# Kernel tuning notes

Measured on AMD Instinct MI355X. Metric: run time of the kernel, lower is better.

## Reference

```python
import jax, jax.numpy as jnp
import numpy as np
from jax import lax

B, C, H, W = 64, 384, 28, 28
E, K, R = 3, 2, 8          # num_experts, top_k, lora rank
HID = 4 * C                # ConvNeXt MLP hidden
EPS = 1e-6
SCALING = 8.0 / 8.0        # alpha / r


def setup_inputs() -> dict:
    key = jax.random.key(0)
    ks = jax.random.split(key, 18)
    N = B * H * W
    f32 = jnp.float32
    inp = {
        "x": jax.random.normal(ks[0], (B, C, H, W), f32),
        "conv_w": jax.random.normal(ks[1], (C, 1, 7, 7), f32) * 0.05,
        "conv_b": jax.random.normal(ks[2], (C,), f32) * 0.02,
        "norm_g": 1.0 + jax.random.normal(ks[3], (C,), f32) * 0.02,
        "norm_b": jax.random.normal(ks[4], (C,), f32) * 0.02,
        "dom_g": jax.random.normal(ks[5], (E, C), f32) * 0.02,
        "dom_b": jax.random.normal(ks[6], (E, C), f32) * 0.02,
        "fc1_w": jax.random.normal(ks[7], (C, HID), f32) * (C ** -0.5),
        "fc1_b": jax.random.normal(ks[8], (HID,), f32) * 0.02,
        "fc2_w": jax.random.normal(ks[9], (HID, C), f32) * (HID ** -0.5),
        "fc2_b": jax.random.normal(ks[10], (C,), f32) * 0.02,
        "w_down": jax.random.normal(ks[11], (E, C, R), f32) * (C ** -0.5),
        "w_up": jax.random.normal(ks[12], (E, R, C), f32) * 0.02,
        "gamma": jax.random.normal(ks[13], (C,), f32) * 0.1,
        "routing_weights": jax.nn.softmax(jax.random.normal(ks[14], (B, E), f32), axis=-1),
        "topk_probs": jax.nn.softmax(jax.random.normal(ks[15], (N, K), f32), axis=-1),
        "topk_indices": jax.random.randint(ks[16], (N, K), 0, E),
    }
    return inp


def _forward(x, conv_w, conv_b, norm_g, norm_b, dom_g, dom_b,
             fc1_w, fc1_b, fc2_w, fc2_b, w_down, w_up, gamma,
             routing_weights, topk_probs, topk_indices):
    shortcut = x
    # depthwise 7x7 conv, NCHW, SAME padding
    y = lax.conv_general_dilated(
        x, conv_w, window_strides=(1, 1), padding=((3, 3), (3, 3)),
        feature_group_count=C,
        dimension_numbers=("NCHW", "OIHW", "NCHW"))
    y = y + conv_b[None, :, None, None]
    y = jnp.transpose(y, (0, 2, 3, 1))  # [B, H, W, C] channels-last path

    # ParallelMoELayerNorm: orig LN + sum_i w_i * LN_i(x). All LNs share eps,
    # so normalize once and fuse affine params per-sample.
    mu = jnp.mean(y, axis=-1, keepdims=True)
    var = jnp.mean(jnp.square(y - mu), axis=-1, keepdims=True)
    xhat = (y - mu) * lax.rsqrt(var + EPS)
    g_eff = norm_g[None, :] + routing_weights @ dom_g   # [B, C]
    b_eff = norm_b[None, :] + routing_weights @ dom_b   # [B, C]
    y = xhat * g_eff[:, None, None, :] + b_eff[:, None, None, :]

    # base ConvNeXt MLP (exact GELU, as torch nn.GELU)
    h = jax.nn.gelu(jnp.einsum("bhwc,cf->bhwf", y, fc1_w) + fc1_b,
                    approximate=False)
    orig_out = jnp.einsum("bhwf,fc->bhwc", h, fc2_w) + fc2_b

    # MoE LoRA: dense per-expert rank-8 compute, combined with top-k weights.
    # Equivalent math to the gather/matmul/scatter-add loop in the source.
    y_flat = y.reshape(-1, C)                                   # [N, C]
    down = jnp.einsum("nc,ecr->enr", y_flat, w_down)            # [E, N, R]
    up = jnp.einsum("enr,erc->enc", jax.nn.gelu(down, approximate=False), w_up)
    # combine weights: comb[n, e] = sum_k topk_probs[n, k] * (topk_indices[n,k]==e)
    comb = jnp.sum(jax.nn.one_hot(topk_indices, E, dtype=y.dtype)
                   * topk_probs[..., None], axis=1)             # [N, E]
    moe_out = jnp.einsum("enc,ne->nc", up * SCALING, comb)
    y = orig_out + moe_out.reshape(B, H, W, C)

    y = jnp.transpose(y, (0, 3, 1, 2))  # back to NCHW
    y = gamma[None, :, None, None] * y  # layer scale; drop_path = identity (eval)
    return y + shortcut


def reference(x, conv_w, conv_b, norm_g, norm_b, dom_g, dom_b,
              fc1_w, fc1_b, fc2_w, fc2_b, w_down, w_up, gamma,
              routing_weights, topk_probs, topk_indices):
    return _forward(x, conv_w, conv_b, norm_g, norm_b, dom_g, dom_b,
                    fc1_w, fc1_b, fc2_w, fc2_b, w_down, w_up, gamma,
                    routing_weights, topk_probs, topk_indices)
```

## Files before the change

kernel.cpp:

```cpp
#include <hip/hip_runtime.h>
#include <hip/hip_bf16.h>
#include <cstdint>
#include <cstddef>

constexpr int cB   = 64;
constexpr int cC   = 384;
constexpr int cH   = 28;
constexpr int cW   = 28;
constexpr int cHID = 1536;
constexpr int cNTOK = cB * cH * cW;
constexpr int cKP   = cHID + 32;
constexpr int cCH   = 2;
constexpr int cMR   = cNTOK / cCH;

typedef __attribute__((ext_vector_type(8))) short bf16x8;
typedef __attribute__((ext_vector_type(4))) float f32x4;

__device__ __forceinline__ float gelu_f(float x) {
  float u = 1.5957691216057308f * x * (1.0f + 0.044715f * x * x);
  float e = __expf(-u);
  return x / (1.0f + e);
}

__device__ __forceinline__ float bf16_to_f(unsigned short s) {
  return __uint_as_float(((unsigned)s) << 16);
}
__device__ __forceinline__ unsigned short f_to_bf16(float v) {
  __hip_bfloat16 hb = __float2bfloat16(v);
  return *reinterpret_cast<unsigned short*>(&hb);
}

__device__ __forceinline__ void gload_lds16(const void* g, void* l) {
  __builtin_amdgcn_global_load_lds(
      (const __attribute__((address_space(1))) unsigned int*)g,
      (__attribute__((address_space(3))) unsigned int*)l, 16, 0, 0);
}

__device__ __forceinline__ int xcd_remap(int b, int nwg) {
  int qn = nwg >> 3, rm = nwg & 7;
  int xcd = b & 7, off = b >> 3;
  return (xcd < rm) ? xcd * (qn + 1) + off
                    : rm * (qn + 1) + (xcd - rm) * qn + off;
}

__global__ __launch_bounds__(256) void prep_eff(
    const float* __restrict__ ng, const float* __restrict__ nb,
    const float* __restrict__ dg, const float* __restrict__ db,
    const float* __restrict__ rw, float* __restrict__ geff, float* __restrict__ beff) {
  int i = blockIdx.x * 256 + threadIdx.x;
  if (i >= cB * cC) return;
  int b = i / cC, c = i - b * cC;
  float g = ng[c], bb = nb[c];
#pragma unroll
  for (int e = 0; e < 3; ++e) {
    float r = rw[b * 3 + e];
    g += r * dg[e * cC + c];
    bb += r * db[e * cC + c];
  }
  geff[i] = g;
  beff[i] = bb;
}

__global__ __launch_bounds__(256) void transpose_bf16(
    const float* __restrict__ w, __hip_bfloat16* __restrict__ wt, int R0, int C0) {
  __shared__ float t[64][65];
  int c0 = blockIdx.x * 64, r0 = blockIdx.y * 64;
  for (int i = threadIdx.x; i < 64 * 64; i += 256) {
    int r = i >> 6, c = i & 63;
    t[r][c] = w[(size_t)(r0 + r) * C0 + c0 + c];
  }
  __syncthreads();
  for (int i = threadIdx.x; i < 64 * 64; i += 256) {
    int c = i >> 6, r = i & 63;
    wt[(size_t)(c0 + c) * R0 + r0 + r] = __float2bfloat16(t[r][c]);
  }
}

__global__ __launch_bounds__(256) void build_fc2t(
    const float* __restrict__ fc2w, const float* __restrict__ wu,
    __hip_bfloat16* __restrict__ fc2t) {
  int i = blockIdx.x * 256 + threadIdx.x;
  if (i >= cC * cKP) return;
  int c = i / cKP, k = i - c * cKP;
  float v = 0.f;
  if (k < cHID) v = fc2w[(size_t)k * cC + c];
  else {
    int j = k - cHID;
    if (j < 24) v = wu[(size_t)(j >> 3) * 8 * cC + (size_t)(j & 7) * cC + c];
  }
  fc2t[i] = __float2bfloat16(v);
}

__global__ __launch_bounds__(256) void build_wdt(
    const float* __restrict__ wd, __hip_bfloat16* __restrict__ wdt) {
  int i = blockIdx.x * 256 + threadIdx.x;
  if (i >= 32 * cC) return;
  int j = i / cC, c = i - j * cC;
  float v = 0.f;
  if (j < 24) v = wd[(size_t)(j >> 3) * cC * 8 + (size_t)c * 8 + (j & 7)];
  wdt[i] = __float2bfloat16(v);
}

constexpr int cPL = 4;
__global__ __launch_bounds__(128) void conv_dw(
    const float* __restrict__ x, const float* __restrict__ cw,
    const float* __restrict__ cb, __hip_bfloat16* __restrict__ out) {
  int pb = blockIdx.x * cPL;
  int c0 = pb % cC;
  __shared__ __align__(16) float tile[cPL][34][38];
  __shared__ float wsm[cPL][49];
  const int tid = threadIdx.x;

  float2 z2 = {0.f, 0.f};
  for (int i = tid; i < cPL * 34 * 38 / 2; i += 128)
    ((float2*)tile)[i] = z2;
  __syncthreads();

  for (int i = tid; i < cPL * 196; i += 128) {
    int p = i / 196, q = i - p * 196;
    int r = q / 7, cl = (q - r * 7) * 4;
    float4 v = *(const float4*)&x[(size_t)(pb + p) * 784 + r * 28 + cl];
    float* dst = &tile[p][r + 3][cl + 4];
    *(float2*)dst = make_float2(v.x, v.y);
    *(float2*)(dst + 2) = make_float2(v.z, v.w);
  }
  for (int i = tid; i < cPL * 49; i += 128) {
    int p = i / 49, k = i - p * 49;
    wsm[p][k] = cw[(size_t)(c0 + p) * 49 + k];
  }
  __syncthreads();

  if (tid < cPL * 28) {
    int p = tid / 28, r = tid - p * 28;
    float acc[28];
    float cbv = cb[c0 + p];
#pragma unroll
    for (int w = 0; w < 28; ++w) acc[w] = cbv;
    for (int dh = 0; dh < 7; ++dh) {
      float rowv[36];
      const float* rp = &tile[p][r + dh][0];
#pragma unroll
      for (int k = 0; k < 18; ++k)
        ((float2*)rowv)[k] = *(const float2*)(rp + k * 2);
      float w7[7];
#pragma unroll
      for (int dw = 0; dw < 7; ++dw) w7[dw] = wsm[p][dh * 7 + dw];
#pragma unroll
      for (int w = 0; w < 28; ++w)
#pragma unroll
        for (int dw = 0; dw < 7; ++dw)
          acc[w] += rowv[w + dw + 1] * w7[dw];
    }
    unsigned short* op = (unsigned short*)out + (size_t)(pb + p) * 784 + r * 28;
#pragma unroll
    for (int k = 0; k < 7; ++k) {
      ushort4 s;
      s.x = f_to_bf16(acc[k * 4 + 0]);
      s.y = f_to_bf16(acc[k * 4 + 1]);
      s.z = f_to_bf16(acc[k * 4 + 2]);
      s.w = f_to_bf16(acc[k * 4 + 3]);
      *(ushort4*)&op[k * 4] = s;
    }
  }
}

__global__ __launch_bounds__(256) void ln_affine(
    const __hip_bfloat16* __restrict__ convout, const float* __restrict__ geff,
    const float* __restrict__ beff, __hip_bfloat16* __restrict__ y) {
  int bh = blockIdx.x;
  int b = bh / cH;
  int hrow = bh - b * cH;
  __shared__ float t[cC * 29];
  const unsigned short* src =
      (const unsigned short*)convout + (size_t)b * cC * (cH * cW) + (size_t)hrow * cW;
  for (int i = threadIdx.x; i < cC * 7; i += 256) {
    int c = i / 7, wq = (i - c * 7) * 4;
    ushort4 v = *(const ushort4*)&src[(size_t)c * (cH * cW) + wq];
    t[c * 29 + wq + 0] = bf16_to_f(v.x);
    t[c * 29 + wq + 1] = bf16_to_f(v.y);
    t[c * 29 + wq + 2] = bf16_to_f(v.z);
    t[c * 29 + wq + 3] = bf16_to_f(v.w);
  }
  __syncthreads();
  int wave = threadIdx.x >> 6, lane = threadIdx.x & 63;
  const float* gp = geff + (size_t)b * cC;
  const float* bp = beff + (size_t)b * cC;
  for (int w = wave; w < cW; w += 4) {
    float v[6], s = 0.f, s2 = 0.f;
#pragma unroll
    for (int j = 0; j < 6; ++j) {
      v[j] = t[(lane + 64 * j) * 29 + w];
      s += v[j];
      s2 += v[j] * v[j];
    }
#pragma unroll
    for (int d = 32; d; d >>= 1) {
      s += __shfl_xor(s, d);
      s2 += __shfl_xor(s2, d);
    }
    float mu = s * (1.0f / cC);
    float var = s2 * (1.0f / cC) - mu * mu;
    float rstd = rsqrtf(var + 1e-6f);
    size_t n = (size_t)bh * cW + w;
#pragma unroll
    for (int j = 0; j < 6; ++j) {
      int c = lane + 64 * j;
      float val = (v[j] - mu) * rstd * gp[c] + bp[c];
      y[n * cC + c] = __float2bfloat16(val);
    }
  }
}

template <int DO_GELU>
__global__ __launch_bounds__(256) void gemm_bt(
    const __hip_bfloat16* __restrict__ A, int lda,
    const __hip_bfloat16* __restrict__ Bt,
    const float* __restrict__ bias,
    __hip_bfloat16* __restrict__ Cb, int ldc,
    int M, int N, int K, int NT_N) {
  __shared__ __align__(16) __hip_bfloat16 As[2][128 * 32];
  __shared__ __align__(16) __hip_bfloat16 Bs[2][128 * 32];

  const int bid = xcd_remap(blockIdx.x, gridDim.x);
  const int gsz = 8 * NT_N;
  const int g = bid / gsz;
  const int q = bid - g * gsz;
  const int mi = g * 8 + q / NT_N;
  const int ni = q - (q / NT_N) * NT_N;
  const int m0 = mi * 128, n0 = ni * 128;

  const int tid = threadIdx.x;
  const int lane = tid & 63;
  const int wid = tid >> 6;
  const int wm = wid >> 1, wn = wid & 1;

  const int base0 = wid * 2048;
  const int base1 = base0 + 1024;
  const int off0 = base0 + lane * 16, off1 = base1 + lane * 16;
  const int row0 = off0 >> 6, col0 = (off0 >> 1) & 31;
  const int row1 = off1 >> 6, col1 = (off1 >> 1) & 31;
  const __hip_bfloat16* pa0 = &A[(size_t)(m0 + row0) * lda + col0];
  const __hip_bfloat16* pa1 = &A[(size_t)(m0 + row1) * lda + col1];
  const __hip_bfloat16* pb0 = &Bt[(size_t)(n0 + row0) * K + col0];
  const __hip_bfloat16* pb1 = &Bt[(size_t)(n0 + row1) * K + col1];

  const int nt = K >> 5;

  gload_lds16(pa0, (char*)As[0] + base0);
  gload_lds16(pa1, (char*)As[0] + base1);
  gload_lds16(pb0, (char*)Bs[0] + base0);
  gload_lds16(pb1, (char*)Bs[0] + base1);
  pa0 += 32; pa1 += 32; pb0 += 32; pb1 += 32;
  __syncthreads();

  f32x4 acc[4][4] = {};
  int cur = 0;
  for (int t = 0; t < nt; ++t, cur ^= 1) {
    if (t + 1 < nt) {
      gload_lds16(pa0, (char*)As[cur ^ 1] + base0);
      gload_lds16(pa1, (char*)As[cur ^ 1] + base1);
      gload_lds16(pb0, (char*)Bs[cur ^ 1] + base0);
      gload_lds16(pb1, (char*)Bs[cur ^ 1] + base1);
      pa0 += 32; pa1 += 32; pb0 += 32; pb1 += 32;
    }
    bf16x8 af[4], bfr[4];
#pragma unroll
    for (int i = 0; i < 4; ++i)
      af[i] = *(const bf16x8*)&As[cur][(wm * 64 + i * 16 + (lane & 15)) * 32 + (lane >> 4) * 8];
#pragma unroll
    for (int i = 0; i < 4; ++i)
      bfr[i] = *(const bf16x8*)&Bs[cur][(wn * 64 + i * 16 + (lane & 15)) * 32 + (lane >> 4) * 8];
#pragma unroll
    for (int i = 0; i < 4; ++i)
#pragma unroll
      for (int j = 0; j < 4; ++j)
        acc[i][j] = __builtin_amdgcn_mfma_f32_16x16x32_bf16(af[i], bfr[j], acc[i][j], 0, 0, 0);
    __syncthreads();
  }

#pragma unroll
  for (int i = 0; i < 4; ++i) {
    int row = m0 + wm * 64 + i * 16 + (lane >> 4) * 4;
#pragma unroll
    for (int j = 0; j < 4; ++j) {
      int col = n0 + wn * 64 + j * 16 + (lane & 15);
      float bv = bias[col];
#pragma unroll
      for (int r = 0; r < 4; ++r) {
        float vv = acc[i][j][r] + bv;
        if (DO_GELU) vv = gelu_f(vv);
        Cb[(size_t)(row + r) * ldc + col] = __float2bfloat16(vv);
      }
    }
  }
}

__global__ __launch_bounds__(256) void lora_down(
    const __hip_bfloat16* __restrict__ y,
    const __hip_bfloat16* __restrict__ wdt,
    const float* __restrict__ probs,
    const int* __restrict__ inds,
    __hip_bfloat16* __restrict__ h) {
  __shared__ __align__(16) __hip_bfloat16 As[2][128 * 32];
  __shared__ __align__(16) __hip_bfloat16 Bsm[32 * 384];
  const int tid = threadIdx.x, lane = tid & 63, wid = tid >> 6;
  const int n0 = blockIdx.x * 128;

  for (int i = tid; i < 32 * 384 / 8; i += 256)
    ((bf16x8*)Bsm)[i] = ((const bf16x8*)wdt)[i];

  const int base0 = wid * 2048, base1 = base0 + 1024;
  const int off0 = base0 + lane * 16, off1 = base1 + lane * 16;
  const int row0 = off0 >> 6, col0 = (off0 >> 1) & 31;
  const int row1 = off1 >> 6, col1 = (off1 >> 1) & 31;
  const __hip_bfloat16* pa0 = &y[(size_t)(n0 + row0) * cC + col0];
  const __hip_bfloat16* pa1 = &y[(size_t)(n0 + row1) * cC + col1];

  const int nt = cC >> 5;
  gload_lds16(pa0, (char*)As[0] + base0);
  gload_lds16(pa1, (char*)As[0] + base1);
  pa0 += 32; pa1 += 32;
  __syncthreads();

  f32x4 acc[2][2] = {};
  int cur = 0;
  for (int t = 0; t < nt; ++t, cur ^= 1) {
    if (t + 1 < nt) {
      gload_lds16(pa0, (char*)As[cur ^ 1] + base0);
      gload_lds16(pa1, (char*)As[cur ^ 1] + base1);
      pa0 += 32; pa1 += 32;
    }
    int kt = t * 32;
    bf16x8 af[2], bfr[2];
#pragma unroll
    for (int i = 0; i < 2; ++i)
      af[i] = *(const bf16x8*)&As[cur][(wid * 32 + i * 16 + (lane & 15)) * 32 + (lane >> 4) * 8];
#pragma unroll
    for (int j = 0; j < 2; ++j)
      bfr[j] = *(const bf16x8*)&Bsm[(j * 16 + (lane & 15)) * 384 + kt + (lane >> 4) * 8];
#pragma unroll
    for (int i = 0; i < 2; ++i)
#pragma unroll
      for (int j = 0; j < 2; ++j)
        acc[i][j] = __builtin_amdgcn_mfma_f32_16x16x32_bf16(af[i], bfr[j], acc[i][j], 0, 0, 0);
    __syncthreads();
  }

#pragma unroll
  for (int i = 0; i < 2; ++i) {
#pragma unroll
    for (int j = 0; j < 2; ++j) {
      int colb = j * 16 + (lane & 15);
#pragma unroll
      for (int r = 0; r < 4; ++r) {
        int n = n0 + wid * 32 + i * 16 + (lane >> 4) * 4 + r;
        float zv = 0.f;
        if (colb < 24) {
          int e = colb >> 3;
          float comb = 0.f;
          if (inds[(size_t)n * 2] == e)     comb += probs[(size_t)n * 2];
          if (inds[(size_t)n * 2 + 1] == e) comb += probs[(size_t)n * 2 + 1];
          zv = comb * gelu_f(acc[i][j][r]);
        }
        h[(size_t)n * cKP + cHID + colb] = __float2bfloat16(zv);
      }
    }
  }
}

__global__ __launch_bounds__(256) void final_out(
    const __hip_bfloat16* __restrict__ tmp, const float* __restrict__ x,
    const float* __restrict__ gamma, float* __restrict__ out) {
  int bh = blockIdx.x;
  int b = bh / cH, hrow = bh - b * cH;
  __shared__ float t[cW * 385];
  const __hip_bfloat16* src = tmp + (size_t)bh * cW * cC;
  for (int i = threadIdx.x; i < cW * cC / 8; i += 256) {
    bf16x8 v = ((const bf16x8*)src)[i];
    int base = i * 8;
    int w = base / cC, c = base - w * cC;
#pragma unroll
    for (int k = 0; k < 8; ++k)
      t[w * 385 + c + k] = bf16_to_f((unsigned short)v[k]);
  }
  __syncthreads();
  const float* xb = x + (size_t)b * cC * (cH * cW) + (size_t)hrow * cW;
  float* ob = out + (size_t)b * cC * (cH * cW) + (size_t)hrow * cW;
  for (int i = threadIdx.x; i < cC * cW; i += 256) {
    int c = i / cW, w = i - c * cW;
    ob[(size_t)c * (cH * cW) + w] = gamma[c] * t[w * 385 + c] + xb[(size_t)c * (cH * cW) + w];
  }
}

extern "C" void kernel_launch(void* const* d_in, const int* in_sizes, int n_in,
                              void* d_out, int out_size, void* d_ws, size_t ws_size,
                              hipStream_t stream) {
  const float* x      = (const float*)d_in[0];
  const float* conv_w = (const float*)d_in[1];
  const float* conv_b = (const float*)d_in[2];
  const float* norm_g = (const float*)d_in[3];
  const float* norm_b = (const float*)d_in[4];
  const float* dom_g  = (const float*)d_in[5];
  const float* dom_b  = (const float*)d_in[6];
  const float* fc1_w  = (const float*)d_in[7];
  const float* fc1_b  = (const float*)d_in[8];
  const float* fc2_w  = (const float*)d_in[9];
  const float* fc2_b  = (const float*)d_in[10];
  const float* w_down = (const float*)d_in[11];
  const float* w_up   = (const float*)d_in[12];
  const float* gamma  = (const float*)d_in[13];
  const float* rw     = (const float*)d_in[14];
  const float* tkp    = (const float*)d_in[15];
  const int*   tki    = (const int*)d_in[16];
  float* out = (float*)d_out;

  char* ws = (char*)d_ws;
  __hip_bfloat16* y      = (__hip_bfloat16*)(ws + 0);
  __hip_bfloat16* tmpb   = (__hip_bfloat16*)(ws + 38535168);
  char*           hslot  = ws + 77070336;
  __hip_bfloat16* h      = (__hip_bfloat16*)hslot;
  __hip_bfloat16* convb  = (__hip_bfloat16*)hslot;
  __hip_bfloat16* fc1t   = (__hip_bfloat16*)(ws + 155746304);
  __hip_bfloat16* fc2t   = (__hip_bfloat16*)(ws + 156925952);
  __hip_bfloat16* wdt    = (__hip_bfloat16*)(ws + 158130176);
  float*          geff   = (float*)(ws + 158154752);
  float*          beff   = (float*)(ws + 158253056);

  prep_eff<<<(cB * cC + 255) / 256, 256, 0, stream>>>(norm_g, norm_b, dom_g, dom_b, rw, geff, beff);
  transpose_bf16<<<dim3(cHID / 64, cC / 64), 256, 0, stream>>>(fc1_w, fc1t, cC, cHID);
  build_fc2t<<<(cC * cKP + 255) / 256, 256, 0, stream>>>(fc2_w, w_up, fc2t);
  build_wdt<<<(32 * cC + 255) / 256, 256, 0, stream>>>(w_down, wdt);
  conv_dw<<<cB * cC / cPL, 128, 0, stream>>>(x, conv_w, conv_b, convb);
  ln_affine<<<cB * cH, 256, 0, stream>>>(convb, geff, beff, y);

  const int NTM = cMR / 128;
  for (int ch = 0; ch < cCH; ++ch) {
    const __hip_bfloat16* ych = y + (size_t)ch * cMR * cC;
    gemm_bt<1><<<NTM * (cHID / 128), 256, 0, stream>>>(
        ych, cC, fc1t, fc1_b, h, cKP, cMR, cHID, cC, cHID / 128);
    lora_down<<<NTM, 256, 0, stream>>>(
        ych, wdt, tkp + (size_t)ch * cMR * 2, tki + (size_t)ch * cMR * 2, h);
    gemm_bt<0><<<NTM * (cC / 128), 256, 0, stream>>>(
        h, cKP, fc2t, fc2_b, tmpb + (size_t)ch * cMR * cC, cC, cMR, cC, cKP, cC / 128);
  }

  final_out<<<cB * cH, 256, 0, stream>>>(tmpb, x, gamma, out);
}
```

Before: 405.2 us.

## Triple-buffer GEMM LDS tiles with explicit vmcnt waits and barriers

Moves the bf16 MFMA GEMM from double to triple buffering of the A/B LDS tiles, so loads run two K-steps ahead. It replaces __syncthreads with partial s_waitcnt vmcnt waits plus raw s_barrier calls, letting one stage's loads stay in flight across the barrier. This aims to hide global-to-LDS latency better. In exchange LDS use grows from 32KB to 48KB per block, which may cut occupancy, and the hand-written wait counts have to match the number of outstanding loads exactly to stay correct.

```diff
diff --git a/kernel.cpp b/kernel.cpp
--- a/kernel.cpp
+++ b/kernel.cpp
@@ -218,8 +218,8 @@
     const float* __restrict__ bias,
     __hip_bfloat16* __restrict__ Cb, int ldc,
     int M, int N, int K, int NT_N) {
-  __shared__ __align__(16) __hip_bfloat16 As[2][128 * 32];
-  __shared__ __align__(16) __hip_bfloat16 Bs[2][128 * 32];
+  __shared__ __align__(16) __hip_bfloat16 As[3][128 * 32];
+  __shared__ __align__(16) __hip_bfloat16 Bs[3][128 * 32];
 
   const int bid = xcd_remap(blockIdx.x, gridDim.x);
   const int gsz = 8 * NT_N;
@@ -246,23 +246,27 @@
 
   const int nt = K >> 5;
 
-  gload_lds16(pa0, (char*)As[0] + base0);
-  gload_lds16(pa1, (char*)As[0] + base1);
-  gload_lds16(pb0, (char*)Bs[0] + base0);
-  gload_lds16(pb1, (char*)Bs[0] + base1);
-  pa0 += 32; pa1 += 32; pb0 += 32; pb1 += 32;
-  __syncthreads();
+#define STAGE(BUF)                                        \
+  do {                                                    \
+    gload_lds16(pa0, (char*)As[BUF] + base0);             \
+    gload_lds16(pa1, (char*)As[BUF] + base1);             \
+    gload_lds16(pb0, (char*)Bs[BUF] + base0);             \
+    gload_lds16(pb1, (char*)Bs[BUF] + base1);             \
+    pa0 += 32; pa1 += 32; pb0 += 32; pb1 += 32;           \
+  } while (0)
+
+  STAGE(0);
+  STAGE(1);
+  asm volatile("s_waitcnt vmcnt(4)" ::: "memory");
+  __builtin_amdgcn_sched_barrier(0);
+  __builtin_amdgcn_s_barrier();
+  __builtin_amdgcn_sched_barrier(0);
 
   f32x4 acc[4][4] = {};
-  int cur = 0;
-  for (int t = 0; t < nt; ++t, cur ^= 1) {
-    if (t + 1 < nt) {
-      gload_lds16(pa0, (char*)As[cur ^ 1] + base0);
-      gload_lds16(pa1, (char*)As[cur ^ 1] + base1);
-      gload_lds16(pb0, (char*)Bs[cur ^ 1] + base0);
-      gload_lds16(pb1, (char*)Bs[cur ^ 1] + base1);
-      pa0 += 32; pa1 += 32; pb0 += 32; pb1 += 32;
-    }
+  int cur = 0, nxt2 = 2;
+  for (int t = 0; t < nt; ++t) {
+    if (t + 2 < nt) STAGE(nxt2);
+
     bf16x8 af[4], bfr[4];
 #pragma unroll
     for (int i = 0; i < 4; ++i)
@@ -275,8 +279,21 @@
 #pragma unroll
       for (int j = 0; j < 4; ++j)
         acc[i][j] = __builtin_amdgcn_mfma_f32_16x16x32_bf16(af[i], bfr[j], acc[i][j], 0, 0, 0);
-    __syncthreads();
-  }
+
+    if (t + 2 < nt) {
+      asm volatile("s_waitcnt vmcnt(4)" ::: "memory");
+    } else if (t + 1 < nt) {
+      asm volatile("s_waitcnt vmcnt(0)" ::: "memory");
+    }
+    if (t + 1 < nt) {
+      __builtin_amdgcn_sched_barrier(0);
+      __builtin_amdgcn_s_barrier();
+      __builtin_amdgcn_sched_barrier(0);
+    }
+    cur = (cur == 2) ? 0 : cur + 1;
+    nxt2 = (nxt2 == 2) ? 0 : nxt2 + 1;
+  }
+#undef STAGE
 
 #pragma unroll
   for (int i = 0; i < 4; ++i) {
```

New measurement: 417.3 us. 1.03x slower.

## Swizzle GEMM LDS tiles, stage epilogue through LDS, run MLP unchunked

Applied to the files above, without the earlier changes.

The GEMM now loads tiles into a single shared buffer with an XOR swizzle on 16-byte chunks, so the MFMA fragment reads avoid LDS bank conflicts. The epilogue writes bias+GELU results to LDS and then stores 16-byte bf16 vectors, replacing scattered 2-byte global stores. The two-chunk token loop is merged into one launch per GEMM over all tokens, which needs a larger hidden buffer and workspace offsets moved to fit it. The K padding grows to 64 and lora_down zero-fills the extra columns, adding a little extra work and memory traffic to fc2.

```diff
diff --git a/kernel.cpp b/kernel.cpp
--- a/kernel.cpp
+++ b/kernel.cpp
@@ -9,9 +9,7 @@
 constexpr int cW   = 28;
 constexpr int cHID = 1536;
 constexpr int cNTOK = cB * cH * cW;
-constexpr int cKP   = cHID + 32;
-constexpr int cCH   = 2;
-constexpr int cMR   = cNTOK / cCH;
+constexpr int cKP   = cHID + 64;
 
 typedef __attribute__((ext_vector_type(8))) short bf16x8;
 typedef __attribute__((ext_vector_type(4))) float f32x4;
@@ -218,9 +216,7 @@
     const float* __restrict__ bias,
     __hip_bfloat16* __restrict__ Cb, int ldc,
     int M, int N, int K, int NT_N) {
-  __shared__ __align__(16) __hip_bfloat16 As[2][128 * 32];
-  __shared__ __align__(16) __hip_bfloat16 Bs[2][128 * 32];
-
+  __shared__ __align__(16) char smem[40960];
   const int bid = xcd_remap(blockIdx.x, gridDim.x);
   const int gsz = 8 * NT_N;
   const int g = bid / gsz;
@@ -233,64 +229,95 @@
   const int lane = tid & 63;
   const int wid = tid >> 6;
   const int wm = wid >> 1, wn = wid & 1;
-
-  const int base0 = wid * 2048;
-  const int base1 = base0 + 1024;
-  const int off0 = base0 + lane * 16, off1 = base1 + lane * 16;
-  const int row0 = off0 >> 6, col0 = (off0 >> 1) & 31;
-  const int row1 = off1 >> 6, col1 = (off1 >> 1) & 31;
-  const __hip_bfloat16* pa0 = &A[(size_t)(m0 + row0) * lda + col0];
-  const __hip_bfloat16* pa1 = &A[(size_t)(m0 + row1) * lda + col1];
-  const __hip_bfloat16* pb0 = &Bt[(size_t)(n0 + row0) * K + col0];
-  const __hip_bfloat16* pb1 = &Bt[(size_t)(n0 + row1) * K + col1];
+  const int l15 = lane & 15, lq = lane >> 4;
+
+  const __hip_bfloat16* srcA[2];
+  const __hip_bfloat16* srcB[2];
+  int dstA[2], dstB[2];
+#pragma unroll
+  for (int a = 0; a < 2; ++a) {
+    int gu = a * 256 + tid;
+    int row = gu >> 2, pu = gu & 3;
+    int u = pu ^ (row & 3);
+    srcA[a] = &A[(size_t)(m0 + row) * lda + u * 8];
+    srcB[a] = &Bt[(size_t)(n0 + row) * K + u * 8];
+    dstA[a] = gu * 16;
+    dstB[a] = 16384 + gu * 16;
+  }
+
+#define STAGE(BUF)                                                   \
+  do {                                                               \
+    _Pragma("unroll") for (int a = 0; a < 2; ++a) {                  \
+      gload_lds16(srcA[a], smem + (BUF) * 8192 + dstA[a]);           \
+      gload_lds16(srcB[a], smem + (BUF) * 8192 + dstB[a]);           \
+      srcA[a] += 32; srcB[a] += 32;                                  \
+    }                                                                \
+  } while (0)
+
+  int roA[4], roB[4];
+#pragma unroll
+  for (int i = 0; i < 4; ++i) {
+    int rowA = wm * 64 + i * 16 + l15;
+    int rowB = wn * 64 + i * 16 + l15;
+    roA[i] = rowA * 64 + (lq ^ (rowA & 3)) * 16;
+    roB[i] = 16384 + rowB * 64 + (lq ^ (rowB & 3)) * 16;
+  }
 
   const int nt = K >> 5;
 
-  gload_lds16(pa0, (char*)As[0] + base0);
-  gload_lds16(pa1, (char*)As[0] + base1);
-  gload_lds16(pb0, (char*)Bs[0] + base0);
-  gload_lds16(pb1, (char*)Bs[0] + base1);
-  pa0 += 32; pa1 += 32; pb0 += 32; pb1 += 32;
+  STAGE(0);
   __syncthreads();
 
   f32x4 acc[4][4] = {};
   int cur = 0;
   for (int t = 0; t < nt; ++t, cur ^= 1) {
-    if (t + 1 < nt) {
-      gload_lds16(pa0, (char*)As[cur ^ 1] + base0);
-      gload_lds16(pa1, (char*)As[cur ^ 1] + base1);
-      gload_lds16(pb0, (char*)Bs[cur ^ 1] + base0);
-      gload_lds16(pb1, (char*)Bs[cur ^ 1] + base1);
-      pa0 += 32; pa1 += 32; pb0 += 32; pb1 += 32;
-    }
-    bf16x8 af[4], bfr[4];
+    if (t + 1 < nt) STAGE(cur ^ 1);
+    const char* base = smem + cur * 8192;
+    bf16x8 af[4], bf[4];
+#pragma unroll
+    for (int i = 0; i < 4; ++i) af[i] = *(const bf16x8*)(base + roA[i]);
+#pragma unroll
+    for (int i = 0; i < 4; ++i) bf[i] = *(const bf16x8*)(base + roB[i]);
 #pragma unroll
     for (int i = 0; i < 4; ++i)
-      af[i] = *(const bf16x8*)&As[cur][(wm * 64 + i * 16 + (lane & 15)) * 32 + (lane >> 4) * 8];
-#pragma unroll
-    for (int i = 0; i < 4; ++i)
-      bfr[i] = *(const bf16x8*)&Bs[cur][(wn * 64 + i * 16 + (lane & 15)) * 32 + (lane >> 4) * 8];
-#pragma unroll
-    for (int i = 0; i < 4; ++i)
 #pragma unroll
       for (int j = 0; j < 4; ++j)
-        acc[i][j] = __builtin_amdgcn_mfma_f32_16x16x32_bf16(af[i], bfr[j], acc[i][j], 0, 0, 0);
+        acc[i][j] = __builtin_amdgcn_mfma_f32_16x16x32_bf16(af[i], bf[j], acc[i][j], 0, 0, 0);
     __syncthreads();
   }
-
-#pragma unroll
-  for (int i = 0; i < 4; ++i) {
-    int row = m0 + wm * 64 + i * 16 + (lane >> 4) * 4;
-#pragma unroll
-    for (int j = 0; j < 4; ++j) {
-      int col = n0 + wn * 64 + j * 16 + (lane & 15);
-      float bv = bias[col];
-#pragma unroll
-      for (int r = 0; r < 4; ++r) {
-        float vv = acc[i][j][r] + bv;
-        if (DO_GELU) vv = gelu_f(vv);
-        Cb[(size_t)(row + r) * ldc + col] = __float2bfloat16(vv);
+#undef STAGE
+
+  float* cst = (float*)smem;
+  for (int hf = 0; hf < 2; ++hf) {
+    if (hf) __syncthreads();
+    if (wn == hf) {
+#pragma unroll
+      for (int i = 0; i < 4; ++i) {
+        int row = wm * 64 + i * 16 + lq * 4;
+#pragma unroll
+        for (int j = 0; j < 4; ++j) {
+          int col = j * 16 + l15;
+          float bv = bias[n0 + hf * 64 + col];
+#pragma unroll
+          for (int r = 0; r < 4; ++r) {
+            float vv = acc[i][j][r] + bv;
+            if (DO_GELU) vv = gelu_f(vv);
+            cst[(row + r) * 72 + col] = vv;
+          }
+        }
       }
+    }
+    __syncthreads();
+#pragma unroll
+    for (int s = 0; s < 4; ++s) {
+      int slot = s * 256 + tid;
+      int row = slot >> 3, c8 = slot & 7;
+      const float* rp = &cst[row * 72 + c8 * 8];
+      bf16x8 v;
+#pragma unroll
+      for (int e = 0; e < 8; ++e)
+        v[e] = (short)f_to_bf16(rp[e]);
+      *(bf16x8*)&Cb[(size_t)(m0 + row) * ldc + n0 + hf * 64 + c8 * 8] = v;
     }
   }
 }
@@ -363,6 +390,7 @@
           zv = comb * gelu_f(acc[i][j][r]);
         }
         h[(size_t)n * cKP + cHID + colb] = __float2bfloat16(zv);
+        h[(size_t)n * cKP + cHID + 32 + colb] = __float2bfloat16(0.f);
       }
     }
   }
@@ -420,11 +448,11 @@
   char*           hslot  = ws + 77070336;
   __hip_bfloat16* h      = (__hip_bfloat16*)hslot;
   __hip_bfloat16* convb  = (__hip_bfloat16*)hslot;
-  __hip_bfloat16* fc1t   = (__hip_bfloat16*)(ws + 155746304);
-  __hip_bfloat16* fc2t   = (__hip_bfloat16*)(ws + 156925952);
-  __hip_bfloat16* wdt    = (__hip_bfloat16*)(ws + 158130176);
-  float*          geff   = (float*)(ws + 158154752);
-  float*          beff   = (float*)(ws + 158253056);
+  __hip_bfloat16* fc1t   = (__hip_bfloat16*)(ws + 237633536);
+  __hip_bfloat16* fc2t   = (__hip_bfloat16*)(ws + 238813184);
+  __hip_bfloat16* wdt    = (__hip_bfloat16*)(ws + 240041984);
+  float*          geff   = (float*)(ws + 240066560);
+  float*          beff   = (float*)(ws + 240164864);
 
   prep_eff<<<(cB * cC + 255) / 256, 256, 0, stream>>>(norm_g, norm_b, dom_g, dom_b, rw, geff, beff);
   transpose_bf16<<<dim3(cHID / 64, cC / 64), 256, 0, stream>>>(fc1_w, fc1t, cC, cHID);
@@ -433,16 +461,12 @@
   conv_dw<<<cB * cC / cPL, 128, 0, stream>>>(x, conv_w, conv_b, convb);
   ln_affine<<<cB * cH, 256, 0, stream>>>(convb, geff, beff, y);
 
-  const int NTM = cMR / 128;
-  for (int ch = 0; ch < cCH; ++ch) {
-    const __hip_bfloat16* ych = y + (size_t)ch * cMR * cC;
-    gemm_bt<1><<<NTM * (cHID / 128), 256, 0, stream>>>(
-        ych, cC, fc1t, fc1_b, h, cKP, cMR, cHID, cC, cHID / 128);
-    lora_down<<<NTM, 256, 0, stream>>>(
-        ych, wdt, tkp + (size_t)ch * cMR * 2, tki + (size_t)ch * cMR * 2, h);
-    gemm_bt<0><<<NTM * (cC / 128), 256, 0, stream>>>(
-        h, cKP, fc2t, fc2_b, tmpb + (size_t)ch * cMR * cC, cC, cMR, cC, cKP, cC / 128);
-  }
+  const int NTM = cNTOK / 128;
+  gemm_bt<1><<<NTM * (cHID / 128), 256, 0, stream>>>(
+      y, cC, fc1t, fc1_b, h, cKP, cNTOK, cHID, cC, cHID / 128);
+  lora_down<<<cNTOK / 128, 256, 0, stream>>>(y, wdt, tkp, tki, h);
+  gemm_bt<0><<<NTM * (cC / 128), 256, 0, stream>>>(
+      h, cKP, fc2t, fc2_b, tmpb, cC, cNTOK, cC, cKP, cC / 128);
 
   final_out<<<cB * cH, 256, 0, stream>>>(tmpb, x, gamma, out);
 }
```

After: 451.8 us. 1.11x slower.

## Fuse layer-scale residual into fc2 GEMM epilogue and swap fc1 operand roles

Applied to the files above, without the earlier changes.

The fc2 GEMM epilogue now applies bias, gamma and the residual add and writes the NCHW fp32 output directly with float4 stores along tokens. This removes the separate final_out kernel and the bf16 intermediate buffer round trip. The fc1 GEMM is rewritten with weights as the M operand and tokens as N, so each lane holds four consecutive hidden units and can load the bias and store h as vectors. Risks: a float4 group of four tokens could cross an image boundary, since 784 is divisible by 4, so this looks safe. The output stores now stride by channel, which may coalesce less well than before.

```diff
diff --git a/kernel.cpp b/kernel.cpp
--- a/kernel.cpp
+++ b/kernel.cpp
@@ -7,6 +7,7 @@
 constexpr int cC   = 384;
 constexpr int cH   = 28;
 constexpr int cW   = 28;
+constexpr int cHW  = cH * cW;
 constexpr int cHID = 1536;
 constexpr int cNTOK = cB * cH * cW;
 constexpr int cKP   = cHID + 32;
@@ -112,7 +113,7 @@
   const int tid = threadIdx.x;
 
   float2 z2 = {0.f, 0.f};
-  for (int i = tid; i < cPL * 34 * 38 / 2; i += 128)
+  for (int i = tid; i < cPL * 34 * 19; i += 128)
     ((float2*)tile)[i] = z2;
   __syncthreads();
 
@@ -172,10 +173,10 @@
   int hrow = bh - b * cH;
   __shared__ float t[cC * 29];
   const unsigned short* src =
-      (const unsigned short*)convout + (size_t)b * cC * (cH * cW) + (size_t)hrow * cW;
+      (const unsigned short*)convout + (size_t)b * cC * cHW + (size_t)hrow * cW;
   for (int i = threadIdx.x; i < cC * 7; i += 256) {
     int c = i / 7, wq = (i - c * 7) * 4;
-    ushort4 v = *(const ushort4*)&src[(size_t)c * (cH * cW) + wq];
+    ushort4 v = *(const ushort4*)&src[(size_t)c * cHW + wq];
     t[c * 29 + wq + 0] = bf16_to_f(v.x);
     t[c * 29 + wq + 1] = bf16_to_f(v.y);
     t[c * 29 + wq + 2] = bf16_to_f(v.z);
@@ -211,16 +212,14 @@
   }
 }
 
-template <int DO_GELU>
-__global__ __launch_bounds__(256) void gemm_bt(
-    const __hip_bfloat16* __restrict__ A, int lda,
-    const __hip_bfloat16* __restrict__ Bt,
+__global__ __launch_bounds__(256) void gemm_fc1(
+    const __hip_bfloat16* __restrict__ Wt,
+    const __hip_bfloat16* __restrict__ Y,
     const float* __restrict__ bias,
-    __hip_bfloat16* __restrict__ Cb, int ldc,
-    int M, int N, int K, int NT_N) {
+    __hip_bfloat16* __restrict__ h) {
   __shared__ __align__(16) __hip_bfloat16 As[2][128 * 32];
   __shared__ __align__(16) __hip_bfloat16 Bs[2][128 * 32];
-
+  const int NT_N = cMR / 128;
   const int bid = xcd_remap(blockIdx.x, gridDim.x);
   const int gsz = 8 * NT_N;
   const int g = bid / gsz;
@@ -233,18 +232,19 @@
   const int lane = tid & 63;
   const int wid = tid >> 6;
   const int wm = wid >> 1, wn = wid & 1;
+  const int l15 = lane & 15, lq = lane >> 4;
 
   const int base0 = wid * 2048;
   const int base1 = base0 + 1024;
   const int off0 = base0 + lane * 16, off1 = base1 + lane * 16;
   const int row0 = off0 >> 6, col0 = (off0 >> 1) & 31;
   const int row1 = off1 >> 6, col1 = (off1 >> 1) & 31;
-  const __hip_bfloat16* pa0 = &A[(size_t)(m0 + row0) * lda + col0];
-  const __hip_bfloat16* pa1 = &A[(size_t)(m0 + row1) * lda + col1];
-  const __hip_bfloat16* pb0 = &Bt[(size_t)(n0 + row0) * K + col0];
-  const __hip_bfloat16* pb1 = &Bt[(size_t)(n0 + row1) * K + col1];
-
-  const int nt = K >> 5;
+  const __hip_bfloat16* pa0 = &Wt[(size_t)(m0 + row0) * cC + col0];
+  const __hip_bfloat16* pa1 = &Wt[(size_t)(m0 + row1) * cC + col1];
+  const __hip_bfloat16* pb0 = &Y[(size_t)(n0 + row0) * cC + col0];
+  const __hip_bfloat16* pb1 = &Y[(size_t)(n0 + row1) * cC + col1];
+
+  const int nt = cC >> 5;
 
   gload_lds16(pa0, (char*)As[0] + base0);
   gload_lds16(pa1, (char*)As[0] + base1);
@@ -263,34 +263,124 @@
       gload_lds16(pb1, (char*)Bs[cur ^ 1] + base1);
       pa0 += 32; pa1 += 32; pb0 += 32; pb1 += 32;
     }
-    bf16x8 af[4], bfr[4];
+    bf16x8 af[4], bf[4];
 #pragma unroll
     for (int i = 0; i < 4; ++i)
-      af[i] = *(const bf16x8*)&As[cur][(wm * 64 + i * 16 + (lane & 15)) * 32 + (lane >> 4) * 8];
+      af[i] = *(const bf16x8*)&As[cur][(wm * 64 + i * 16 + l15) * 32 + lq * 8];
 #pragma unroll
     for (int i = 0; i < 4; ++i)
-      bfr[i] = *(const bf16x8*)&Bs[cur][(wn * 64 + i * 16 + (lane & 15)) * 32 + (lane >> 4) * 8];
+      bf[i] = *(const bf16x8*)&Bs[cur][(wn * 64 + i * 16 + l15) * 32 + lq * 8];
 #pragma unroll
     for (int i = 0; i < 4; ++i)
 #pragma unroll
       for (int j = 0; j < 4; ++j)
-        acc[i][j] = __builtin_amdgcn_mfma_f32_16x16x32_bf16(af[i], bfr[j], acc[i][j], 0, 0, 0);
+        acc[i][j] = __builtin_amdgcn_mfma_f32_16x16x32_bf16(af[i], bf[j], acc[i][j], 0, 0, 0);
     __syncthreads();
   }
 
 #pragma unroll
   for (int i = 0; i < 4; ++i) {
-    int row = m0 + wm * 64 + i * 16 + (lane >> 4) * 4;
+    int hid = m0 + wm * 64 + i * 16 + lq * 4;
+    float4 bv = *(const float4*)&bias[hid];
 #pragma unroll
     for (int j = 0; j < 4; ++j) {
-      int col = n0 + wn * 64 + j * 16 + (lane & 15);
-      float bv = bias[col];
-#pragma unroll
-      for (int r = 0; r < 4; ++r) {
-        float vv = acc[i][j][r] + bv;
-        if (DO_GELU) vv = gelu_f(vv);
-        Cb[(size_t)(row + r) * ldc + col] = __float2bfloat16(vv);
-      }
+      int tok = n0 + wn * 64 + j * 16 + l15;
+      ushort4 s;
+      s.x = f_to_bf16(gelu_f(acc[i][j][0] + bv.x));
+      s.y = f_to_bf16(gelu_f(acc[i][j][1] + bv.y));
+      s.z = f_to_bf16(gelu_f(acc[i][j][2] + bv.z));
+      s.w = f_to_bf16(gelu_f(acc[i][j][3] + bv.w));
+      *(ushort4*)&h[(size_t)tok * cKP + hid] = s;
+    }
+  }
+}
+
+__global__ __launch_bounds__(256) void gemm_fc2o(
+    const __hip_bfloat16* __restrict__ Hc,
+    const __hip_bfloat16* __restrict__ Bt,
+    const float* __restrict__ bias,
+    const float* __restrict__ gamma,
+    const float* __restrict__ x,
+    float* __restrict__ out,
+    int tok0) {
+  __shared__ __align__(16) __hip_bfloat16 As[2][128 * 32];
+  __shared__ __align__(16) __hip_bfloat16 Bs[2][128 * 32];
+  const int NT_N = cC / 128;
+  const int bid = xcd_remap(blockIdx.x, gridDim.x);
+  const int gsz = 8 * NT_N;
+  const int g = bid / gsz;
+  const int q = bid - g * gsz;
+  const int mi = g * 8 + q / NT_N;
+  const int ni = q - (q / NT_N) * NT_N;
+  const int m0 = mi * 128, n0 = ni * 128;
+
+  const int tid = threadIdx.x;
+  const int lane = tid & 63;
+  const int wid = tid >> 6;
+  const int wm = wid >> 1, wn = wid & 1;
+  const int l15 = lane & 15, lq = lane >> 4;
+
+  const int base0 = wid * 2048;
+  const int base1 = base0 + 1024;
+  const int off0 = base0 + lane * 16, off1 = base1 + lane * 16;
+  const int row0 = off0 >> 6, col0 = (off0 >> 1) & 31;
+  const int row1 = off1 >> 6, col1 = (off1 >> 1) & 31;
+  const __hip_bfloat16* pa0 = &Hc[(size_t)(m0 + row0) * cKP + col0];
+  const __hip_bfloat16* pa1 = &Hc[(size_t)(m0 + row1) * cKP + col1];
+  const __hip_bfloat16* pb0 = &Bt[(size_t)(n0 + row0) * cKP + col0];
+  const __hip_bfloat16* pb1 = &Bt[(size_t)(n0 + row1) * cKP + col1];
+
+  const int nt = cKP >> 5;
+
+  gload_lds16(pa0, (char*)As[0] + base0);
+  gload_lds16(pa1, (char*)As[0] + base1);
+  gload_lds16(pb0, (char*)Bs[0] + base0);
+  gload_lds16(pb1, (char*)Bs[0] + base1);
+  pa0 += 32; pa1 += 32; pb0 += 32; pb1 += 32;
+  __syncthreads();
+
+  f32x4 acc[4][4] = {};
+  int cur = 0;
+  for (int t = 0; t < nt; ++t, cur ^= 1) {
+    if (t + 1 < nt) {
+      gload_lds16(pa0, (char*)As[cur ^ 1] + base0);
+      gload_lds16(pa1, (char*)As[cur ^ 1] + base1);
+      gload_lds16(pb0, (char*)Bs[cur ^ 1] + base0);
+      gload_lds16(pb1, (char*)Bs[cur ^ 1] + base1);
+      pa0 += 32; pa1 += 32; pb0 += 32; pb1 += 32;
+    }
+    bf16x8 af[4], bf[4];
+#pragma unroll
+    for (int i = 0; i < 4; ++i)
+      af[i] = *(const bf16x8*)&As[cur][(wm * 64 + i * 16 + l15) * 32 + lq * 8];
+#pragma unroll
+    for (int i = 0; i < 4; ++i)
+      bf[i] = *(const bf16x8*)&Bs[cur][(wn * 64 + i * 16 + l15) * 32 + lq * 8];
+#pragma unroll
+    for (int i = 0; i < 4; ++i)
+#pragma unroll
+      for (int j = 0; j < 4; ++j)
+        acc[i][j] = __builtin_amdgcn_mfma_f32_16x16x32_bf16(af[i], bf[j], acc[i][j], 0, 0, 0);
+    __syncthreads();
+  }
+
+#pragma unroll
+  for (int i = 0; i < 4; ++i) {
+    int tok = tok0 + m0 + wm * 64 + i * 16 + lq * 4;
+    int b = tok / cHW;
+    int hw = tok - b * cHW;
+#pragma unroll
+    for (int j = 0; j < 4; ++j) {
+      int c = n0 + wn * 64 + j * 16 + l15;
+      float bv = bias[c], ga = gamma[c];
+      size_t o = ((size_t)b * cC + c) * cHW + hw;
+      float4 xr = *(const float4*)&x[o];
+      float4 ov;
+      ov.x = ga * (acc[i][j][0] + bv) + xr.x;
+      ov.y = ga * (acc[i][j][1] + bv) + xr.y;
+      ov.z = ga * (acc[i][j][2] + bv) + xr.z;
+      ov.w = ga * (acc[i][j][3] + bv) + xr.w;
+      *(float4*)&out[o] = ov;
     }
   }
 }
@@ -365,30 +455,6 @@
         h[(size_t)n * cKP + cHID + colb] = __float2bfloat16(zv);
       }
     }
-  }
-}
-
-__global__ __launch_bounds__(256) void final_out(
-    const __hip_bfloat16* __restrict__ tmp, const float* __restrict__ x,
-    const float* __restrict__ gamma, float* __restrict__ out) {
-  int bh = blockIdx.x;
-  int b = bh / cH, hrow = bh - b * cH;
-  __shared__ float t[cW * 385];
-  const __hip_bfloat16* src = tmp + (size_t)bh * cW * cC;
-  for (int i = threadIdx.x; i < cW * cC / 8; i += 256) {
-    bf16x8 v = ((const bf16x8*)src)[i];
-    int base = i * 8;
-    int w = base / cC, c = base - w * cC;
-#pragma unroll
-    for (int k = 0; k < 8; ++k)
-      t[w * 385 + c + k] = bf16_to_f((unsigned short)v[k]);
-  }
-  __syncthreads();
-  const float* xb = x + (size_t)b * cC * (cH * cW) + (size_t)hrow * cW;
-  float* ob = out + (size_t)b * cC * (cH * cW) + (size_t)hrow * cW;
-  for (int i = threadIdx.x; i < cC * cW; i += 256) {
-    int c = i / cW, w = i - c * cW;
-    ob[(size_t)c * (cH * cW) + w] = gamma[c] * t[w * 385 + c] + xb[(size_t)c * (cH * cW) + w];
   }
 }
 
@@ -416,15 +482,14 @@
 
   char* ws = (char*)d_ws;
   __hip_bfloat16* y      = (__hip_bfloat16*)(ws + 0);
-  __hip_bfloat16* tmpb   = (__hip_bfloat16*)(ws + 38535168);
-  char*           hslot  = ws + 77070336;
+  char*           hslot  = ws + 38535168;
   __hip_bfloat16* h      = (__hip_bfloat16*)hslot;
   __hip_bfloat16* convb  = (__hip_bfloat16*)hslot;
-  __hip_bfloat16* fc1t   = (__hip_bfloat16*)(ws + 155746304);
-  __hip_bfloat16* fc2t   = (__hip_bfloat16*)(ws + 156925952);
-  __hip_bfloat16* wdt    = (__hip_bfloat16*)(ws + 158130176);
-  float*          geff   = (float*)(ws + 158154752);
-  float*          beff   = (float*)(ws + 158253056);
+  __hip_bfloat16* fc1t   = (__hip_bfloat16*)(ws + 117211136);
+  __hip_bfloat16* fc2t   = (__hip_bfloat16*)(ws + 118390784);
+  __hip_bfloat16* wdt    = (__hip_bfloat16*)(ws + 119595008);
+  float*          geff   = (float*)(ws + 119619584);
+  float*          beff   = (float*)(ws + 119717888);
 
   prep_eff<<<(cB * cC + 255) / 256, 256, 0, stream>>>(norm_g, norm_b, dom_g, dom_b, rw, geff, beff);
   transpose_bf16<<<dim3(cHID / 64, cC / 64), 256, 0, stream>>>(fc1_w, fc1t, cC, cHID);
@@ -436,13 +501,10 @@
   const int NTM = cMR / 128;
   for (int ch = 0; ch < cCH; ++ch) {
     const __hip_bfloat16* ych = y + (size_t)ch * cMR * cC;
-    gemm_bt<1><<<NTM * (cHID / 128), 256, 0, stream>>>(
-        ych, cC, fc1t, fc1_b, h, cKP, cMR, cHID, cC, cHID / 128);
+    gemm_fc1<<<(cHID / 128) * NTM, 256, 0, stream>>>(fc1t, ych, fc1_b, h);
     lora_down<<<NTM, 256, 0, stream>>>(
         ych, wdt, tkp + (size_t)ch * cMR * 2, tki + (size_t)ch * cMR * 2, h);
-    gemm_bt<0><<<NTM * (cC / 128), 256, 0, stream>>>(
-        h, cKP, fc2t, fc2_b, tmpb + (size_t)ch * cMR * cC, cC, cMR, cC, cKP, cC / 128);
-  }
-
-  final_out<<<cB * cH, 256, 0, stream>>>(tmpb, x, gamma, out);
-}
+    gemm_fc2o<<<NTM * (cC / 128), 256, 0, stream>>>(
+        h, fc2t, fc2_b, gamma, x, out, ch * cMR);
+  }
+}
```

After: 485.7 us. +19.9%, slower.
